# Performance work log

Hardware: AMD Instinct MI355X
Metric: run time of the kernel (lower is better)

The kernel has to match this reference:

```python
import jax, jax.numpy as jnp
import numpy as np

BS, N, D, H = 2, 512, 512, 16
DD = D // H
EPS = 1e-5


def _layernorm(h, g, b):
    mu = jnp.mean(h, axis=-1, keepdims=True)
    var = jnp.mean((h - mu) ** 2, axis=-1, keepdims=True)
    return (h - mu) / jnp.sqrt(var + EPS) * g + b


def setup_inputs() -> dict:
    key = jax.random.key(0)
    ks = jax.random.split(key, 10)
    x = jax.random.normal(ks[0], (BS, N, D), dtype=jnp.float32)
    u = jax.random.uniform(ks[1], (BS, N, N), dtype=jnp.float32)
    adj = jnp.where(u > 0.3, u, 0.0)
    s = 0.02
    return {
        "x": x,
        "adj": adj,
        "W_fc": jax.random.normal(ks[2], (D, D), dtype=jnp.float32) * s,
        "b_fc": jnp.zeros((D,), dtype=jnp.float32),
        "W_fc2": jax.random.normal(ks[3], (D, D), dtype=jnp.float32) * s,
        "b_fc2": jnp.zeros((D,), dtype=jnp.float32),
        "W_val": jax.random.normal(ks[4], (D, D), dtype=jnp.float32) * s,
        "b_val": jnp.zeros((D,), dtype=jnp.float32),
        "aff": jax.random.normal(ks[5], (H, DD), dtype=jnp.float32) * s,
        "aff_bias": jnp.zeros((H,), dtype=jnp.float32),
        "ln_g": jnp.ones((D,), dtype=jnp.float32),
        "ln_b": jnp.zeros((D,), dtype=jnp.float32),
        "t": 0,
    }


def reference(x, adj, W_fc, b_fc, W_fc2, b_fc2, W_val, b_val, aff, aff_bias, ln_g, ln_b, t):
    bs, n, d = x.shape
    # projections -> [bs, H, n, dd]
    def proj(W, b):
        return (x @ W.T + b).reshape(bs, n, H, DD).transpose(0, 2, 1, 3)
    x_val = proj(W_val, b_val)
    x_aff = proj(W_fc, b_fc)
    x_aff2 = proj(W_fc2, b_fc2)
    # GAT additive scores: leaky_relu over all (i,j) pairs, then dot with aff
    v = jax.nn.leaky_relu(x_aff[:, :, :, None, :] + x_aff2[:, :, None, :, :], 0.2)  # [bs,H,n,n,dd]
    scores = jnp.einsum('bhijd,hd->bhij', v, aff) + aff_bias[None, :, None, None]
    scores = jnp.where(adj[:, None, :, :] < 1e-5, jnp.float32(-1e9), scores)
    attn = jax.nn.softmax(scores, axis=-1)  # [bs,H,n,n]
    out = jnp.einsum('bhij,bhjd->bhid', attn, x_val)  # [bs,H,n,dd]
    out = out.transpose(0, 2, 1, 3).reshape(bs, n, d)
    x_aff_flat = x_aff.transpose(0, 2, 1, 3).reshape(bs, n, d)
    h = _layernorm(x_aff_flat + out, ln_g, ln_b)
    return jax.nn.relu(h)
```

## Files before the change

### kernel.cpp

```cpp
#include <hip/hip_runtime.h>


#define NB 2
#define NN 512
#define DM 512
#define NH 16
#define DD 32
#define RLOG2E 1.4426950408889634f

typedef __attribute__((ext_vector_type(8))) short bf16x8;
typedef __attribute__((ext_vector_type(4))) float f32x4;
typedef _Float16 h2 __attribute__((ext_vector_type(2)));
typedef _Float16 h8 __attribute__((ext_vector_type(8)));
typedef __fp16 fp16x2 __attribute__((ext_vector_type(2)));

__device__ __forceinline__ h2 u2h(unsigned int u) { union { unsigned int x; h2 h; } c; c.x = u; return c.h; }
__device__ __forceinline__ unsigned int h2u(h2 v) { union { unsigned int x; h2 h; } c; c.h = v; return c.x; }
__device__ __forceinline__ h8 u4h8(uint4 v) { union { uint4 u; h8 h; } c; c.u = v; return c.h; }
__device__ __forceinline__ h2 pkrtz(float x, float y) {
  union { fp16x2 a; h2 b; } c; c.a = __builtin_amdgcn_cvt_pkrtz(x, y); return c.b;
}

#if __has_builtin(__builtin_amdgcn_fdot2)
#define DOT2(a, b, c) __builtin_amdgcn_fdot2((a), (b), (c), false)
#else
#define DOT2(a, b, c) fmaf((float)(a)[0], (float)(b)[0], fmaf((float)(a)[1], (float)(b)[1], (c)))
#endif

__device__ __forceinline__ unsigned short f2bf(float f) {
  unsigned int u = __float_as_uint(f);
  u = (u + 0x7FFFu + ((u >> 16) & 1u)) >> 16;
  return (unsigned short)u;
}

__global__ void prep_kernel(const float* __restrict__ x, const float* __restrict__ w0,
                            const float* __restrict__ w1, const float* __restrict__ w2,
                            const float* __restrict__ adj,
                            unsigned short* __restrict__ xb, unsigned short* __restrict__ wb0,
                            unsigned short* __restrict__ wb1, unsigned short* __restrict__ wb2,
                            unsigned int* __restrict__ bits) {
  int gid = blockIdx.x * 256 + threadIdx.x;
  if (gid < 327680) {
    const float* src; unsigned short* dst; int off;
    if (gid < 131072)      { src = x;  dst = xb;  off = gid; }
    else if (gid < 196608) { src = w0; dst = wb0; off = gid - 131072; }
    else if (gid < 262144) { src = w1; dst = wb1; off = gid - 196608; }
    else                   { src = w2; dst = wb2; off = gid - 262144; }
    float4 v = ((const float4*)src)[off];
    ushort4 r;
    r.x = f2bf(v.x); r.y = f2bf(v.y); r.z = f2bf(v.z); r.w = f2bf(v.w);
    ((ushort4*)dst)[off] = r;
  } else {
    int t = gid - 327680;
    if (t < 16384) {
      int bb = t >> 13, rem = t & 8191;
      int i = rem >> 4, jw = rem & 15;
      const float4* ap = (const float4*)(adj + ((size_t)(bb * NN + i)) * NN + jw * 32);
      unsigned int word = 0;
      #pragma unroll
      for (int q = 0; q < 8; ++q) {
        float4 v = ap[q];
        if (v.x >= 1e-5f) word |= 1u << (q * 4 + 0);
        if (v.y >= 1e-5f) word |= 1u << (q * 4 + 1);
        if (v.z >= 1e-5f) word |= 1u << (q * 4 + 2);
        if (v.w >= 1e-5f) word |= 1u << (q * 4 + 3);
      }
      bits[((bb * 16) + jw) * 512 + i] = word;
    }
  }
}

__global__ void proj_kernel(const unsigned short* __restrict__ xb,
                            const unsigned short* __restrict__ wb0,
                            const unsigned short* __restrict__ wb1,
                            const unsigned short* __restrict__ wb2,
                            const float* __restrict__ bias0, const float* __restrict__ bias1,
                            const float* __restrict__ bias2,
                            _Float16* __restrict__ Pfch, _Float16* __restrict__ Pfc2h,
                            _Float16* __restrict__ Pvalh) {
  const int mt = blockIdx.x, nt = blockIdx.y, which = blockIdx.z;
  const unsigned short* W = (which == 0) ? wb0 : (which == 1) ? wb1 : wb2;
  const float* bias       = (which == 0) ? bias0 : (which == 1) ? bias1 : bias2;
  _Float16* Ph            = (which == 0) ? Pfch : (which == 1) ? Pfc2h : Pvalh;
  const int tid = threadIdx.x;
  const int wv = tid >> 6, lane = tid & 63;
  const int wm = wv >> 1, wn = wv & 1;
  const int mbase = mt * 64 + wm * 32, nbase = nt * 64 + wn * 32;
  const int lr = lane & 15, lk = lane >> 4;
  const bf16x8* A0 = (const bf16x8*)(xb + (size_t)(mbase + lr) * 512 + lk * 8);
  const bf16x8* A1 = (const bf16x8*)(xb + (size_t)(mbase + 16 + lr) * 512 + lk * 8);
  const bf16x8* B0 = (const bf16x8*)(W + (size_t)(nbase + lr) * 512 + lk * 8);
  const bf16x8* B1 = (const bf16x8*)(W + (size_t)(nbase + 16 + lr) * 512 + lk * 8);
  f32x4 acc00 = {0.f, 0.f, 0.f, 0.f}, acc01 = acc00, acc10 = acc00, acc11 = acc00;
  #pragma unroll
  for (int kt = 0; kt < 16; ++kt) {
    bf16x8 a0 = A0[kt * 4], a1 = A1[kt * 4];
    bf16x8 b0 = B0[kt * 4], b1 = B1[kt * 4];
    acc00 = __builtin_amdgcn_mfma_f32_16x16x32_bf16(a0, b0, acc00, 0, 0, 0);
    acc01 = __builtin_amdgcn_mfma_f32_16x16x32_bf16(a0, b1, acc01, 0, 0, 0);
    acc10 = __builtin_amdgcn_mfma_f32_16x16x32_bf16(a1, b0, acc10, 0, 0, 0);
    acc11 = __builtin_amdgcn_mfma_f32_16x16x32_bf16(a1, b1, acc11, 0, 0, 0);
  }
  const int r0 = mbase + lk * 4, c0 = nbase + lr;
  #pragma unroll
  for (int v = 0; v < 4; ++v) {
    Ph[(size_t)(r0 + v) * 512 + c0]           = (_Float16)(acc00[v] + bias[c0]);
    Ph[(size_t)(r0 + v) * 512 + c0 + 16]      = (_Float16)(acc01[v] + bias[c0 + 16]);
    Ph[(size_t)(r0 + 16 + v) * 512 + c0]      = (_Float16)(acc10[v] + bias[c0]);
    Ph[(size_t)(r0 + 16 + v) * 512 + c0 + 16] = (_Float16)(acc11[v] + bias[c0 + 16]);
  }
}

__global__ void aux_kernel(const _Float16* __restrict__ Pfch, const _Float16* __restrict__ Pfc2h,
                           const float* __restrict__ aff,
                           float* __restrict__ sa, float* __restrict__ sb) {
  int gid = blockIdx.x * 256 + threadIdx.x;
  int h = gid & 15, row = gid >> 4;
  const float* ar = aff + h * 32;
  const h2* p1 = (const h2*)(Pfch + (size_t)row * 512 + h * 32);
  const h2* p2 = (const h2*)(Pfc2h + (size_t)row * 512 + h * 32);
  float s1 = 0.f, s2 = 0.f;
  #pragma unroll
  for (int d2 = 0; d2 < 16; ++d2) {
    h2 v1 = p1[d2], v2 = p2[d2];
    float a0 = ar[2 * d2], a1 = ar[2 * d2 + 1];
    s1 = fmaf(a0, (float)v1[0], s1); s1 = fmaf(a1, (float)v1[1], s1);
    s2 = fmaf(a0, (float)v2[0], s2); s2 = fmaf(a1, (float)v2[1], s2);
  }
  int b = row >> 9, i = row & 511;
  int o = (b * NH + h) * NN + i;
  const float sc = 0.6f * RLOG2E;
  sa[o] = s1 * sc; sb[o] = s2 * sc;
}

__launch_bounds__(256)
__global__ void attn_kernel(const _Float16* __restrict__ Pfch,
                            const _Float16* __restrict__ Pfc2h,
                            const _Float16* __restrict__ Pvalh,
                            const float* __restrict__ sa, const float* __restrict__ sb,
                            const float* __restrict__ aff,
                            const unsigned int* __restrict__ bits,
                            float* __restrict__ part_l, _Float16* __restrict__ part_oh) {
  const int bx = blockIdx.x;
  const int it = bx >> 3, jh = bx & 7;
  const int h = blockIdx.y, b = blockIdx.z;
  const int tid = threadIdx.x;
  const int w = tid >> 6, lane = tid & 63;
  const int i0 = it * 128 + lane, i1 = i0 + 64;
  const int jbase = jh * 64;

  __shared__ uint4 Bt4[256];
  __shared__ uint4 VtT4[256];
  __shared__ uint4 Pt4[1024];
  __shared__ float slm[4][128];
  __shared__ float sbt[64];

  {
    const int row = tid >> 2, seg = tid & 3;
    uint4 bv = *(const uint4*)(Pfc2h + ((size_t)(b * NN + jbase + row)) * DM + h * DD + seg * 8);
    Bt4[tid] = bv;
    uint4 vv = *(const uint4*)(Pvalh + ((size_t)(b * NN + jbase + row)) * DM + h * DD + seg * 8);
    _Float16* VtT_h = (_Float16*)VtT4;
    const int jc = row >> 3, jr = row & 7;
    #pragma unroll
    for (int e = 0; e < 4; ++e) {
      h2 pr = u2h(((const unsigned int*)&vv)[e]);
      int d0 = seg * 8 + 2 * e, d1 = d0 + 1;
      VtT_h[d0 * 64 + ((jc ^ (d0 & 7)) * 8) + jr] = pr[0];
      VtT_h[d1 * 64 + ((jc ^ (d1 & 7)) * 8) + jr] = pr[1];
    }
    if (tid < 64) sbt[tid] = sb[(b * NH + h) * NN + jbase + tid];
  }

  h2 a0h[16], a1h[16], afh[16];
  {
    const uint4* ap0 = (const uint4*)(Pfch + ((size_t)(b * NN + i0)) * DM + h * DD);
    const uint4* ap1 = (const uint4*)(Pfch + ((size_t)(b * NN + i1)) * DM + h * DD);
    #pragma unroll
    for (int q = 0; q < 4; ++q) {
      uint4 v0 = ap0[q], v1 = ap1[q];
      a0h[q * 4 + 0] = u2h(v0.x); a0h[q * 4 + 1] = u2h(v0.y);
      a0h[q * 4 + 2] = u2h(v0.z); a0h[q * 4 + 3] = u2h(v0.w);
      a1h[q * 4 + 0] = u2h(v1.x); a1h[q * 4 + 1] = u2h(v1.y);
      a1h[q * 4 + 2] = u2h(v1.z); a1h[q * 4 + 3] = u2h(v1.w);
    }
    const float4* fp = (const float4*)(aff + h * DD);
    const float afs = 0.4f * RLOG2E;
    #pragma unroll
    for (int q = 0; q < 8; ++q) {
      float4 fv = fp[q];
      afh[q * 2 + 0] = pkrtz(fv.x * afs, fv.y * afs);
      afh[q * 2 + 1] = pkrtz(fv.z * afs, fv.w * afs);
    }
  }
  const float sai0 = sa[(b * NH + h) * NN + i0];
  const float sai1 = sa[(b * NH + h) * NN + i1];
  const unsigned int mw0 = bits[((b * 16) + jh * 2 + (w >> 1)) * NN + i0] >> ((w & 1) * 16);
  const unsigned int mw1 = bits[((b * 16) + jh * 2 + (w >> 1)) * NN + i1] >> ((w & 1) * 16);
  float l0 = 0.f, l1 = 0.f;
  h2 ph0[8], ph1[8];

  __syncthreads();

  const int jt0 = w * 16;
  #pragma unroll
  for (int jp = 0; jp < 8; ++jp) {
    float pe0, pe1, po0, po1;
    #pragma unroll
    for (int q = 0; q < 2; ++q) {
      const int jo = jp * 2 + q;
      const int jl = jt0 + jo;
      uint4 bq0 = Bt4[jl * 4 + 0], bq1 = Bt4[jl * 4 + 1];
      uint4 bq2 = Bt4[jl * 4 + 2], bq3 = Bt4[jl * 4 + 3];
      const float sbj = sbt[jl];
      float t00 = 0.f, t01 = 0.f, t10 = 0.f, t11 = 0.f;
      #define SC2(k, dw, T0, T1)                                       \
        { h2 bh = u2h(dw);                                             \
          h2 u0 = u2h(h2u(a0h[k] + bh) & 0x7FFF7FFFu);                 \
          h2 u1 = u2h(h2u(a1h[k] + bh) & 0x7FFF7FFFu);                 \
          T0 = DOT2(afh[k], u0, T0);                                   \
          T1 = DOT2(afh[k], u1, T1); }
      SC2(0,  bq0.x, t00, t10) SC2(1,  bq0.y, t01, t11)
      SC2(2,  bq0.z, t00, t10) SC2(3,  bq0.w, t01, t11)
      SC2(4,  bq1.x, t00, t10) SC2(5,  bq1.y, t01, t11)
      SC2(6,  bq1.z, t00, t10) SC2(7,  bq1.w, t01, t11)
      SC2(8,  bq2.x, t00, t10) SC2(9,  bq2.y, t01, t11)
      SC2(10, bq2.z, t00, t10) SC2(11, bq2.w, t01, t11)
      SC2(12, bq3.x, t00, t10) SC2(13, bq3.y, t01, t11)
      SC2(14, bq3.z, t00, t10) SC2(15, bq3.w, t01, t11)
      #undef SC2
      const float s0 = sai0 + sbj + (t00 + t01);
      const float s1 = sai1 + sbj + (t10 + t11);
      const float p0 = ((mw0 >> jo) & 1u) ? __builtin_amdgcn_exp2f(s0) : 0.f;
      const float p1 = ((mw1 >> jo) & 1u) ? __builtin_amdgcn_exp2f(s1) : 0.f;
      l0 += p0; l1 += p1;
      if (q == 0) { pe0 = p0; pe1 = p1; } else { po0 = p0; po1 = p1; }
    }
    ph0[jp] = pkrtz(pe0, po0);
    ph1[jp] = pkrtz(pe1, po1);
  }

  slm[w][lane] = l0; slm[w][lane + 64] = l1;
  {
    const int c0 = 2 * w, c1 = 2 * w + 1;
    uint4 q00 = make_uint4(h2u(ph0[0]), h2u(ph0[1]), h2u(ph0[2]), h2u(ph0[3]));
    uint4 q01 = make_uint4(h2u(ph0[4]), h2u(ph0[5]), h2u(ph0[6]), h2u(ph0[7]));
    uint4 q10 = make_uint4(h2u(ph1[0]), h2u(ph1[1]), h2u(ph1[2]), h2u(ph1[3]));
    uint4 q11 = make_uint4(h2u(ph1[4]), h2u(ph1[5]), h2u(ph1[6]), h2u(ph1[7]));
    const int r0 = lane, r1 = lane + 64;
    Pt4[r0 * 8 + (c0 ^ (r0 & 7))] = q00;
    Pt4[r0 * 8 + (c1 ^ (r0 & 7))] = q01;
    Pt4[r1 * 8 + (c0 ^ (r1 & 7))] = q10;
    Pt4[r1 * 8 + (c1 ^ (r1 & 7))] = q11;
  }
  __syncthreads();

  {
    const int lr = lane & 15, lk = lane >> 4;
    #pragma unroll
    for (int rti = 0; rti < 2; ++rti) {
      const int rt = w * 2 + rti;
      const int row = rt * 16 + lr;
      uint4 a4_0 = Pt4[row * 8 + ((lk) ^ (row & 7))];
      uint4 a4_1 = Pt4[row * 8 + ((4 + lk) ^ (row & 7))];
      #pragma unroll
      for (int ct = 0; ct < 2; ++ct) {
        const int d = ct * 16 + lr;
        uint4 b4_0 = VtT4[d * 8 + ((lk) ^ (d & 7))];
        uint4 b4_1 = VtT4[d * 8 + ((4 + lk) ^ (d & 7))];
        f32x4 acc = {0.f, 0.f, 0.f, 0.f};
        acc = __builtin_amdgcn_mfma_f32_16x16x32_f16(u4h8(a4_0), u4h8(b4_0), acc, 0, 0, 0);
        acc = __builtin_amdgcn_mfma_f32_16x16x32_f16(u4h8(a4_1), u4h8(b4_1), acc, 0, 0, 0);
        #pragma unroll
        for (int v = 0; v < 4; ++v) {
          const int grow = it * 128 + rt * 16 + lk * 4 + v;
          const size_t prow = (((size_t)(jh * 2 + b) * NH + h) * NN + grow);
          part_oh[prow * 32 + ct * 16 + lr] = (_Float16)acc[v];
        }
      }
    }
    if (tid < 128) {
      const int r = tid;
      const size_t prow = (((size_t)(jh * 2 + b) * NH + h) * NN + it * 128 + r);
      part_l[prow] = (slm[0][r] + slm[1][r]) + (slm[2][r] + slm[3][r]);
    }
  }
}

__global__ void comb_ln_kernel(const unsigned int* __restrict__ part_o,
                               const float* __restrict__ part_l,
                               const _Float16* __restrict__ Pfch,
                               const float* __restrict__ g, const float* __restrict__ be,
                               float* __restrict__ out) {
  const int t = threadIdx.x;
  const int rg = blockIdx.x * 8 + (t >> 5);
  const int b = rg >> 9, i = rg & 511;
  const int l32 = t & 31;
  const int d0 = l32 * 16;
  const int h0 = d0 >> 5;
  const int dh = d0 & 31;
  float o[16];
  #pragma unroll
  for (int k = 0; k < 16; ++k) o[k] = 0.f;
  float L = 0.f;
  #pragma unroll
  for (int s = 0; s < 8; ++s) {
    const size_t prow = (((size_t)(s * 2 + b) * NH + h0) * NN + i);
    L += part_l[prow];
    const uint4* po = (const uint4*)(part_o + prow * 16 + (dh >> 1));
    uint4 q0 = po[0], q1 = po[1];
    #define ACC(k, dw) { h2 hh = u2h(dw); o[2*(k)] += (float)hh[0]; o[2*(k)+1] += (float)hh[1]; }
    ACC(0, q0.x) ACC(1, q0.y) ACC(2, q0.z) ACC(3, q0.w)
    ACC(4, q1.x) ACC(5, q1.y) ACC(6, q1.z) ACC(7, q1.w)
    #undef ACC
  }
  const float inv = 1.f / L;
  const uint4* pfh = (const uint4*)(Pfch + ((size_t)(b * NN + i)) * DM + d0);
  uint4 r0 = pfh[0], r1 = pfh[1];
  float pfv[16];
  #define UNP(k, dw) { h2 hh = u2h(dw); pfv[2*(k)] = (float)hh[0]; pfv[2*(k)+1] = (float)hh[1]; }
  UNP(0, r0.x) UNP(1, r0.y) UNP(2, r0.z) UNP(3, r0.w)
  UNP(4, r1.x) UNP(5, r1.y) UNP(6, r1.z) UNP(7, r1.w)
  #undef UNP
  float hv[16];
  float sS = 0.f, sQ = 0.f;
  #pragma unroll
  for (int k = 0; k < 16; ++k) {
    float hvv = pfv[k] + o[k] * inv;
    hv[k] = hvv;
    sS += hvv;
    sQ = fmaf(hvv, hvv, sQ);
  }
  #pragma unroll
  for (int off = 16; off > 0; off >>= 1) {
    sS += __shfl_xor(sS, off);
    sQ += __shfl_xor(sQ, off);
  }
  const float mu = sS * (1.f / 512.f);
  const float var = sQ * (1.f / 512.f) - mu * mu;
  const float rstd = rsqrtf(var + 1e-5f);
  float4* op = (float4*)(out + ((size_t)(b * NN + i)) * DM + d0);
  #pragma unroll
  for (int k = 0; k < 4; ++k) {
    float4 gv = ((const float4*)(g + d0))[k];
    float4 bv = ((const float4*)(be + d0))[k];
    float4 res;
    res.x = fmaxf((hv[4 * k + 0] - mu) * rstd * gv.x + bv.x, 0.f);
    res.y = fmaxf((hv[4 * k + 1] - mu) * rstd * gv.y + bv.y, 0.f);
    res.z = fmaxf((hv[4 * k + 2] - mu) * rstd * gv.z + bv.z, 0.f);
    res.w = fmaxf((hv[4 * k + 3] - mu) * rstd * gv.w + bv.w, 0.f);
    op[k] = res;
  }
}

extern "C" void kernel_launch(void* const* d_in, const int* in_sizes, int n_in,
                              void* d_out, int out_size, void* d_ws, size_t ws_size,
                              hipStream_t stream) {
  const float* x    = (const float*)d_in[0];
  const float* adj  = (const float*)d_in[1];
  const float* Wfc  = (const float*)d_in[2];
  const float* bfc  = (const float*)d_in[3];
  const float* Wfc2 = (const float*)d_in[4];
  const float* bfc2 = (const float*)d_in[5];
  const float* Wval = (const float*)d_in[6];
  const float* bval = (const float*)d_in[7];
  const float* aff  = (const float*)d_in[8];
  const float* lng  = (const float*)d_in[10];
  const float* lnb  = (const float*)d_in[11];
  float* out = (float*)d_out;

  char* ws = (char*)d_ws;
  unsigned short* xb  = (unsigned short*)(ws);
  unsigned short* wb0 = (unsigned short*)(ws + 1048576);
  unsigned short* wb1 = (unsigned short*)(ws + 1572864);
  unsigned short* wb2 = (unsigned short*)(ws + 2097152);
  _Float16* part_oh = (_Float16*)(ws);
  float* part_l   = (float*)(ws + 8388608);
  _Float16* Pfch  = (_Float16*)(ws + 8912896);
  _Float16* Pfc2h = (_Float16*)(ws + 9961472);
  _Float16* Pvalh = (_Float16*)(ws + 11010048);
  float* sa       = (float*)(ws + 12058624);
  float* sb       = (float*)(ws + 12124160);
  unsigned int* bits = (unsigned int*)(ws + 12189696);

  prep_kernel<<<1344, 256, 0, stream>>>(x, Wfc, Wfc2, Wval, adj, xb, wb0, wb1, wb2, bits);
  proj_kernel<<<dim3(16, 8, 3), 256, 0, stream>>>(xb, wb0, wb1, wb2, bfc, bfc2, bval,
                                                  Pfch, Pfc2h, Pvalh);
  aux_kernel<<<64, 256, 0, stream>>>(Pfch, Pfc2h, aff, sa, sb);
  attn_kernel<<<dim3(32, 16, 2), 256, 0, stream>>>(Pfch, Pfc2h, Pvalh, sa, sb, aff, bits,
                                                   part_l, part_oh);
  comb_ln_kernel<<<128, 256, 0, stream>>>((const unsigned int*)part_oh, part_l, Pfch,
                                          lng, lnb, out);
}
```

Measured before the change: 59.25 us.

## Fuse score-prefix dot into projection epilogue and halve attention rows per block

The aux_kernel that computed the per-row linear score terms sa/sb is removed; the projection kernel now computes them in its epilogue from the fp32 accumulators, using a 16-lane shuffle reduction, which saves one launch and a reread of the projections. The attention kernel now handles 64 query rows per block instead of 128, so the grid doubles to 2048 blocks with one row per thread. This lowers register and LDS pressure and adds parallelism, at the cost of reloading the shared B/V tiles twice as often. The sa/sb values now come from unrounded fp32 accumulators rather than the fp16-stored projections, which slightly changes rounding.

```diff
diff --git a/kernel.cpp b/kernel.cpp
--- a/kernel.cpp
+++ b/kernel.cpp
@@ -76,8 +76,10 @@
                             const unsigned short* __restrict__ wb2,
                             const float* __restrict__ bias0, const float* __restrict__ bias1,
                             const float* __restrict__ bias2,
+                            const float* __restrict__ aff,
                             _Float16* __restrict__ Pfch, _Float16* __restrict__ Pfc2h,
-                            _Float16* __restrict__ Pvalh) {
+                            _Float16* __restrict__ Pvalh,
+                            float* __restrict__ sa, float* __restrict__ sb) {
   const int mt = blockIdx.x, nt = blockIdx.y, which = blockIdx.z;
   const unsigned short* W = (which == 0) ? wb0 : (which == 1) ? wb1 : wb2;
   const float* bias       = (which == 0) ? bias0 : (which == 1) ? bias1 : bias2;
@@ -101,36 +103,44 @@
     acc10 = __builtin_amdgcn_mfma_f32_16x16x32_bf16(a1, b0, acc10, 0, 0, 0);
     acc11 = __builtin_amdgcn_mfma_f32_16x16x32_bf16(a1, b1, acc11, 0, 0, 0);
   }
-  const int r0 = mbase + lk * 4, c0 = nbase + lr;
+  const int r0 = mbase + lk * 4, cb = nbase + lr;
+  const int hw = nt * 2 + wn;
+  const float afA = aff[hw * 32 + lr];
+  const float afB = aff[hw * 32 + lr + 16];
+  float pa[4], pb[4];
   #pragma unroll
   for (int v = 0; v < 4; ++v) {
-    Ph[(size_t)(r0 + v) * 512 + c0]           = (_Float16)(acc00[v] + bias[c0]);
-    Ph[(size_t)(r0 + v) * 512 + c0 + 16]      = (_Float16)(acc01[v] + bias[c0 + 16]);
-    Ph[(size_t)(r0 + 16 + v) * 512 + c0]      = (_Float16)(acc10[v] + bias[c0]);
-    Ph[(size_t)(r0 + 16 + v) * 512 + c0 + 16] = (_Float16)(acc11[v] + bias[c0 + 16]);
-  }
-}
-
-__global__ void aux_kernel(const _Float16* __restrict__ Pfch, const _Float16* __restrict__ Pfc2h,
-                           const float* __restrict__ aff,
-                           float* __restrict__ sa, float* __restrict__ sb) {
-  int gid = blockIdx.x * 256 + threadIdx.x;
-  int h = gid & 15, row = gid >> 4;
-  const float* ar = aff + h * 32;
-  const h2* p1 = (const h2*)(Pfch + (size_t)row * 512 + h * 32);
-  const h2* p2 = (const h2*)(Pfc2h + (size_t)row * 512 + h * 32);
-  float s1 = 0.f, s2 = 0.f;
-  #pragma unroll
-  for (int d2 = 0; d2 < 16; ++d2) {
-    h2 v1 = p1[d2], v2 = p2[d2];
-    float a0 = ar[2 * d2], a1 = ar[2 * d2 + 1];
-    s1 = fmaf(a0, (float)v1[0], s1); s1 = fmaf(a1, (float)v1[1], s1);
-    s2 = fmaf(a0, (float)v2[0], s2); s2 = fmaf(a1, (float)v2[1], s2);
-  }
-  int b = row >> 9, i = row & 511;
-  int o = (b * NH + h) * NN + i;
-  const float sc = 0.6f * RLOG2E;
-  sa[o] = s1 * sc; sb[o] = s2 * sc;
+    float r00 = acc00[v] + bias[cb];
+    float r01 = acc01[v] + bias[cb + 16];
+    float r10 = acc10[v] + bias[cb];
+    float r11 = acc11[v] + bias[cb + 16];
+    Ph[(size_t)(r0 + v) * 512 + cb]           = (_Float16)r00;
+    Ph[(size_t)(r0 + v) * 512 + cb + 16]      = (_Float16)r01;
+    Ph[(size_t)(r0 + 16 + v) * 512 + cb]      = (_Float16)r10;
+    Ph[(size_t)(r0 + 16 + v) * 512 + cb + 16] = (_Float16)r11;
+    pa[v] = fmaf(afA, r00, afB * r01);
+    pb[v] = fmaf(afA, r10, afB * r11);
+  }
+  if (which < 2) {
+    #pragma unroll
+    for (int m = 1; m < 16; m <<= 1) {
+      #pragma unroll
+      for (int v = 0; v < 4; ++v) {
+        pa[v] += __shfl_xor(pa[v], m);
+        pb[v] += __shfl_xor(pb[v], m);
+      }
+    }
+    if (lr == 0) {
+      float* dst = (which == 0) ? sa : sb;
+      const float sc = 0.6f * RLOG2E;
+      #pragma unroll
+      for (int v = 0; v < 4; ++v) {
+        int g0 = r0 + v, g1 = r0 + 16 + v;
+        dst[((g0 >> 9) * NH + hw) * NN + (g0 & 511)] = pa[v] * sc;
+        dst[((g1 >> 9) * NH + hw) * NN + (g1 & 511)] = pb[v] * sc;
+      }
+    }
+  }
 }
 
 __launch_bounds__(256)
@@ -146,13 +156,13 @@
   const int h = blockIdx.y, b = blockIdx.z;
   const int tid = threadIdx.x;
   const int w = tid >> 6, lane = tid & 63;
-  const int i0 = it * 128 + lane, i1 = i0 + 64;
+  const int i = it * 64 + lane;
   const int jbase = jh * 64;
 
   __shared__ uint4 Bt4[256];
   __shared__ uint4 VtT4[256];
-  __shared__ uint4 Pt4[1024];
-  __shared__ float slm[4][128];
+  __shared__ uint4 Pt4[512];
+  __shared__ float slm[4][64];
   __shared__ float sbt[64];
 
   {
@@ -172,17 +182,14 @@
     if (tid < 64) sbt[tid] = sb[(b * NH + h) * NN + jbase + tid];
   }
 
-  h2 a0h[16], a1h[16], afh[16];
+  h2 ah[16], afh[16];
   {
-    const uint4* ap0 = (const uint4*)(Pfch + ((size_t)(b * NN + i0)) * DM + h * DD);
-    const uint4* ap1 = (const uint4*)(Pfch + ((size_t)(b * NN + i1)) * DM + h * DD);
+    const uint4* ap = (const uint4*)(Pfch + ((size_t)(b * NN + i)) * DM + h * DD);
     #pragma unroll
     for (int q = 0; q < 4; ++q) {
-      uint4 v0 = ap0[q], v1 = ap1[q];
-      a0h[q * 4 + 0] = u2h(v0.x); a0h[q * 4 + 1] = u2h(v0.y);
-      a0h[q * 4 + 2] = u2h(v0.z); a0h[q * 4 + 3] = u2h(v0.w);
-      a1h[q * 4 + 0] = u2h(v1.x); a1h[q * 4 + 1] = u2h(v1.y);
-      a1h[q * 4 + 2] = u2h(v1.z); a1h[q * 4 + 3] = u2h(v1.w);
+      uint4 v0 = ap[q];
+      ah[q * 4 + 0] = u2h(v0.x); ah[q * 4 + 1] = u2h(v0.y);
+      ah[q * 4 + 2] = u2h(v0.z); ah[q * 4 + 3] = u2h(v0.w);
     }
     const float4* fp = (const float4*)(aff + h * DD);
     const float afs = 0.4f * RLOG2E;
@@ -193,96 +200,78 @@
       afh[q * 2 + 1] = pkrtz(fv.z * afs, fv.w * afs);
     }
   }
-  const float sai0 = sa[(b * NH + h) * NN + i0];
-  const float sai1 = sa[(b * NH + h) * NN + i1];
-  const unsigned int mw0 = bits[((b * 16) + jh * 2 + (w >> 1)) * NN + i0] >> ((w & 1) * 16);
-  const unsigned int mw1 = bits[((b * 16) + jh * 2 + (w >> 1)) * NN + i1] >> ((w & 1) * 16);
-  float l0 = 0.f, l1 = 0.f;
-  h2 ph0[8], ph1[8];
+  const float sai = sa[(b * NH + h) * NN + i];
+  const unsigned int mw = bits[((b * 16) + jh * 2 + (w >> 1)) * NN + i] >> ((w & 1) * 16);
+  float l = 0.f;
+  h2 ph[8];
 
   __syncthreads();
 
   const int jt0 = w * 16;
   #pragma unroll
   for (int jp = 0; jp < 8; ++jp) {
-    float pe0, pe1, po0, po1;
+    float pv2[2];
     #pragma unroll
     for (int q = 0; q < 2; ++q) {
       const int jo = jp * 2 + q;
       const int jl = jt0 + jo;
       uint4 bq0 = Bt4[jl * 4 + 0], bq1 = Bt4[jl * 4 + 1];
       uint4 bq2 = Bt4[jl * 4 + 2], bq3 = Bt4[jl * 4 + 3];
-      const float sbj = sbt[jl];
-      float t00 = 0.f, t01 = 0.f, t10 = 0.f, t11 = 0.f;
-      #define SC2(k, dw, T0, T1)                                       \
-        { h2 bh = u2h(dw);                                             \
-          h2 u0 = u2h(h2u(a0h[k] + bh) & 0x7FFF7FFFu);                 \
-          h2 u1 = u2h(h2u(a1h[k] + bh) & 0x7FFF7FFFu);                 \
-          T0 = DOT2(afh[k], u0, T0);                                   \
-          T1 = DOT2(afh[k], u1, T1); }
-      SC2(0,  bq0.x, t00, t10) SC2(1,  bq0.y, t01, t11)
-      SC2(2,  bq0.z, t00, t10) SC2(3,  bq0.w, t01, t11)
-      SC2(4,  bq1.x, t00, t10) SC2(5,  bq1.y, t01, t11)
-      SC2(6,  bq1.z, t00, t10) SC2(7,  bq1.w, t01, t11)
-      SC2(8,  bq2.x, t00, t10) SC2(9,  bq2.y, t01, t11)
-      SC2(10, bq2.z, t00, t10) SC2(11, bq2.w, t01, t11)
-      SC2(12, bq3.x, t00, t10) SC2(13, bq3.y, t01, t11)
-      SC2(14, bq3.z, t00, t10) SC2(15, bq3.w, t01, t11)
+      float t0 = 0.f, t1 = 0.f;
+      #define SC2(k, dw, T)                                          \
+        { h2 bh = u2h(dw);                                           \
+          h2 u0 = u2h(h2u(ah[k] + bh) & 0x7FFF7FFFu);                \
+          T = DOT2(afh[k], u0, T); }
+      SC2(0,  bq0.x, t0) SC2(1,  bq0.y, t1)
+      SC2(2,  bq0.z, t0) SC2(3,  bq0.w, t1)
+      SC2(4,  bq1.x, t0) SC2(5,  bq1.y, t1)
+      SC2(6,  bq1.z, t0) SC2(7,  bq1.w, t1)
+      SC2(8,  bq2.x, t0) SC2(9,  bq2.y, t1)
+      SC2(10, bq2.z, t0) SC2(11, bq2.w, t1)
+      SC2(12, bq3.x, t0) SC2(13, bq3.y, t1)
+      SC2(14, bq3.z, t0) SC2(15, bq3.w, t1)
       #undef SC2
-      const float s0 = sai0 + sbj + (t00 + t01);
-      const float s1 = sai1 + sbj + (t10 + t11);
-      const float p0 = ((mw0 >> jo) & 1u) ? __builtin_amdgcn_exp2f(s0) : 0.f;
-      const float p1 = ((mw1 >> jo) & 1u) ? __builtin_amdgcn_exp2f(s1) : 0.f;
-      l0 += p0; l1 += p1;
-      if (q == 0) { pe0 = p0; pe1 = p1; } else { po0 = p0; po1 = p1; }
-    }
-    ph0[jp] = pkrtz(pe0, po0);
-    ph1[jp] = pkrtz(pe1, po1);
-  }
-
-  slm[w][lane] = l0; slm[w][lane + 64] = l1;
+      const float s = sai + sbt[jl] + (t0 + t1);
+      const float p = ((mw >> jo) & 1u) ? __builtin_amdgcn_exp2f(s) : 0.f;
+      l += p;
+      pv2[q] = p;
+    }
+    ph[jp] = pkrtz(pv2[0], pv2[1]);
+  }
+
+  slm[w][lane] = l;
   {
     const int c0 = 2 * w, c1 = 2 * w + 1;
-    uint4 q00 = make_uint4(h2u(ph0[0]), h2u(ph0[1]), h2u(ph0[2]), h2u(ph0[3]));
-    uint4 q01 = make_uint4(h2u(ph0[4]), h2u(ph0[5]), h2u(ph0[6]), h2u(ph0[7]));
-    uint4 q10 = make_uint4(h2u(ph1[0]), h2u(ph1[1]), h2u(ph1[2]), h2u(ph1[3]));
-    uint4 q11 = make_uint4(h2u(ph1[4]), h2u(ph1[5]), h2u(ph1[6]), h2u(ph1[7]));
-    const int r0 = lane, r1 = lane + 64;
-    Pt4[r0 * 8 + (c0 ^ (r0 & 7))] = q00;
-    Pt4[r0 * 8 + (c1 ^ (r0 & 7))] = q01;
-    Pt4[r1 * 8 + (c0 ^ (r1 & 7))] = q10;
-    Pt4[r1 * 8 + (c1 ^ (r1 & 7))] = q11;
+    uint4 q0 = make_uint4(h2u(ph[0]), h2u(ph[1]), h2u(ph[2]), h2u(ph[3]));
+    uint4 q1 = make_uint4(h2u(ph[4]), h2u(ph[5]), h2u(ph[6]), h2u(ph[7]));
+    Pt4[lane * 8 + (c0 ^ (lane & 7))] = q0;
+    Pt4[lane * 8 + (c1 ^ (lane & 7))] = q1;
   }
   __syncthreads();
 
   {
     const int lr = lane & 15, lk = lane >> 4;
-    #pragma unroll
-    for (int rti = 0; rti < 2; ++rti) {
-      const int rt = w * 2 + rti;
-      const int row = rt * 16 + lr;
-      uint4 a4_0 = Pt4[row * 8 + ((lk) ^ (row & 7))];
-      uint4 a4_1 = Pt4[row * 8 + ((4 + lk) ^ (row & 7))];
+    const int row = w * 16 + lr;
+    uint4 a4_0 = Pt4[row * 8 + ((lk) ^ (row & 7))];
+    uint4 a4_1 = Pt4[row * 8 + ((4 + lk) ^ (row & 7))];
+    #pragma unroll
+    for (int ct = 0; ct < 2; ++ct) {
+      const int d = ct * 16 + lr;
+      uint4 b4_0 = VtT4[d * 8 + ((lk) ^ (d & 7))];
+      uint4 b4_1 = VtT4[d * 8 + ((4 + lk) ^ (d & 7))];
+      f32x4 acc = {0.f, 0.f, 0.f, 0.f};
+      acc = __builtin_amdgcn_mfma_f32_16x16x32_f16(u4h8(a4_0), u4h8(b4_0), acc, 0, 0, 0);
+      acc = __builtin_amdgcn_mfma_f32_16x16x32_f16(u4h8(a4_1), u4h8(b4_1), acc, 0, 0, 0);
       #pragma unroll
-      for (int ct = 0; ct < 2; ++ct) {
-        const int d = ct * 16 + lr;
-        uint4 b4_0 = VtT4[d * 8 + ((lk) ^ (d & 7))];
-        uint4 b4_1 = VtT4[d * 8 + ((4 + lk) ^ (d & 7))];
-        f32x4 acc = {0.f, 0.f, 0.f, 0.f};
-        acc = __builtin_amdgcn_mfma_f32_16x16x32_f16(u4h8(a4_0), u4h8(b4_0), acc, 0, 0, 0);
-        acc = __builtin_amdgcn_mfma_f32_16x16x32_f16(u4h8(a4_1), u4h8(b4_1), acc, 0, 0, 0);
-        #pragma unroll
-        for (int v = 0; v < 4; ++v) {
-          const int grow = it * 128 + rt * 16 + lk * 4 + v;
-          const size_t prow = (((size_t)(jh * 2 + b) * NH + h) * NN + grow);
-          part_oh[prow * 32 + ct * 16 + lr] = (_Float16)acc[v];
-        }
+      for (int v = 0; v < 4; ++v) {
+        const int grow = it * 64 + w * 16 + lk * 4 + v;
+        const size_t prow = (((size_t)(jh * 2 + b) * NH + h) * NN + grow);
+        part_oh[prow * 32 + ct * 16 + lr] = (_Float16)acc[v];
       }
     }
-    if (tid < 128) {
-      const int r = tid;
-      const size_t prow = (((size_t)(jh * 2 + b) * NH + h) * NN + it * 128 + r);
-      part_l[prow] = (slm[0][r] + slm[1][r]) + (slm[2][r] + slm[3][r]);
+    if (tid < 64) {
+      const size_t prow = (((size_t)(jh * 2 + b) * NH + h) * NN + it * 64 + tid);
+      part_l[prow] = (slm[0][tid] + slm[1][tid]) + (slm[2][tid] + slm[3][tid]);
     }
   }
 }
@@ -384,10 +373,9 @@
   unsigned int* bits = (unsigned int*)(ws + 12189696);
 
   prep_kernel<<<1344, 256, 0, stream>>>(x, Wfc, Wfc2, Wval, adj, xb, wb0, wb1, wb2, bits);
-  proj_kernel<<<dim3(16, 8, 3), 256, 0, stream>>>(xb, wb0, wb1, wb2, bfc, bfc2, bval,
-                                                  Pfch, Pfc2h, Pvalh);
-  aux_kernel<<<64, 256, 0, stream>>>(Pfch, Pfc2h, aff, sa, sb);
-  attn_kernel<<<dim3(32, 16, 2), 256, 0, stream>>>(Pfch, Pfc2h, Pvalh, sa, sb, aff, bits,
+  proj_kernel<<<dim3(16, 8, 3), 256, 0, stream>>>(xb, wb0, wb1, wb2, bfc, bfc2, bval, aff,
+                                                  Pfch, Pfc2h, Pvalh, sa, sb);
+  attn_kernel<<<dim3(64, 16, 2), 256, 0, stream>>>(Pfch, Pfc2h, Pvalh, sa, sb, aff, bits,
                                                    part_l, part_oh);
   comb_ln_kernel<<<128, 256, 0, stream>>>((const unsigned int*)part_oh, part_l, Pfch,
                                           lng, lnb, out);
```

Result: faster. 56.01 us (-5.5%).
